# Kernel optimization log

Measured on AMD Instinct MI355X. Metric: run time of the kernel, lower is better.

Reference implementation:

```python
import jax, jax.numpy as jnp
import numpy as np

DIM, NH, HD = 512, 16, 32   # dim, num_heads, head_dim = dim // num_heads
WH, WW = 8, 8               # window_size
SCALE = HD ** -0.5


def _rope2(t):
    """Axial 2D rotary embedding. t: (M, WH, WW, HD). First HD/2 dims rotate
    with the height position, last HD/2 with the width position."""
    d = HD // 2
    inv_freq = 1.0 / (10000.0 ** (jnp.arange(0, d, 2, dtype=jnp.float32) / d))  # (d/2,)

    def cos_sin(n):
        ang = jnp.arange(n, dtype=jnp.float32)[:, None] * inv_freq              # (n, d/2)
        return (jnp.concatenate([jnp.cos(ang)] * 2, -1),
                jnp.concatenate([jnp.sin(ang)] * 2, -1))                        # (n, d)

    def rot_half(u):
        u1, u2 = jnp.split(u, 2, axis=-1)
        return jnp.concatenate([-u2, u1], -1)

    cos_h, sin_h = cos_sin(WH)
    cos_w, sin_w = cos_sin(WW)
    th, tw = t[..., :d], t[..., d:]
    th = th * cos_h[:, None, :] + rot_half(th) * sin_h[:, None, :]
    tw = tw * cos_w[None, :, :] + rot_half(tw) * sin_w[None, :, :]
    return jnp.concatenate([th, tw], -1)


def setup_inputs() -> dict:
    key = jax.random.key(0)
    ks = jax.random.split(key, 8)
    s = 0.02
    return {
        "x": jax.random.normal(ks[0], (8, 64, 64, DIM), dtype=jnp.float32),
        "qkv_w": jax.random.normal(ks[1], (DIM, 3 * DIM), dtype=jnp.float32) * s,
        "qkv_b": jnp.zeros((3 * DIM,), dtype=jnp.float32),
        "kv_w": jax.random.normal(ks[2], (DIM, 2 * DIM), dtype=jnp.float32) * s,
        "kv_b": jnp.zeros((2 * DIM,), dtype=jnp.float32),
        "proj_w": jax.random.normal(ks[3], (DIM, DIM), dtype=jnp.float32) * s,
        "proj_b": jnp.zeros((DIM,), dtype=jnp.float32),
    }


def reference(x, qkv_w, qkv_b, kv_w, kv_b, proj_w, proj_b):
    B, H, W, C = x.shape
    # --- hydra linear-attention branch (computed in the torch module even when
    # use_attn=True, but its result is discarded on that path) ---
    hy_k, hy_v = jnp.split(x @ kv_w + kv_b, 2, axis=-1)
    hy_k = hy_k / jnp.linalg.norm(hy_k, axis=-1, keepdims=True)
    hy_kv = (hy_k * hy_v).reshape(B, -1, C).sum(axis=-2, keepdims=True)  # (B,1,C), unused (use_attn=True)

    # --- window partition: (B,H,W,C) -> (B*nW, N, C), N = WH*WW ---
    xw = (x.reshape(B, H // WH, WH, W // WW, WW, C)
           .transpose(0, 1, 3, 2, 4, 5)
           .reshape(-1, WH * WW, C))
    B_, N, _ = xw.shape

    qkv = (xw @ qkv_w + qkv_b).reshape(B_, N, 3, NH, HD).transpose(2, 0, 3, 1, 4)
    q, k, v = qkv[0], qkv[1], qkv[2]                 # each (B_, NH, N, HD)

    q = _rope2(q.reshape(-1, WH, WW, HD)).reshape(B_, NH, N, HD)
    k = _rope2(k.reshape(-1, WH, WW, HD)).reshape(B_, NH, N, HD)

    attn = jax.nn.softmax(jnp.einsum('bhnd,bhmd->bhnm', q * SCALE, k), axis=-1)
    out = jnp.einsum('bhnm,bhmd->bhnd', attn, v)     # (B_, NH, N, HD)
    out = out.transpose(0, 2, 1, 3).reshape(B_, N, C)

    # --- window reverse: (B*nW, N, C) -> (B, H*W, C) ---
    out = (out.reshape(B, H // WH, W // WW, WH, WW, C)
              .transpose(0, 1, 3, 2, 4, 5)
              .reshape(B, H * W, C))

    out = out @ proj_w + proj_b
    return out.reshape(B, H, W, C)
```

## Files before the change

### kernel.cpp

```cpp
#include <hip/hip_runtime.h>
#include <cstdint>
#include <cstddef>

typedef float v4f  __attribute__((ext_vector_type(4)));
typedef __bf16 v8bf __attribute__((ext_vector_type(8)));
typedef __bf16 v4bf __attribute__((ext_vector_type(4)));

#define M_TOT 32768
#define KDIM  512
#define NQKV  1536
#define NPROJ 512

__device__ __constant__ float c_invf[8] = {
  1.f, 0.31622776601683794f, 0.1f, 0.031622776601683794f,
  0.01f, 0.0031622776601683794f, 0.001f, 0.00031622776601683794f };

__device__ __forceinline__ void async_copy16(const void* g, void* l) {
  __builtin_amdgcn_global_load_lds((const __attribute__((address_space(1))) void*)g,
                                   (__attribute__((address_space(3))) void*)l, 16, 0, 0);
}

__global__ void cast_x_kernel(const float* __restrict__ in, __bf16* __restrict__ out, int n8) {
  int i = blockIdx.x * blockDim.x + threadIdx.x;
  if (i >= n8) return;
  const float4* p = (const float4*)in + (size_t)i * 2;
  float4 a = p[0], b = p[1];
  v8bf r = { (__bf16)a.x, (__bf16)a.y, (__bf16)a.z, (__bf16)a.w,
             (__bf16)b.x, (__bf16)b.y, (__bf16)b.z, (__bf16)b.w };
  *(v8bf*)(out + (size_t)i * 8) = r;
}

__global__ __launch_bounds__(256) void transpose_cast_kernel(
    const float* __restrict__ w, __bf16* __restrict__ wt, int K, int N) {
  __shared__ __bf16 t[64 * 72];
  const int tid = threadIdx.x;
  const int n0 = blockIdx.x * 64, k0 = blockIdx.y * 64;
#pragma unroll
  for (int i = 0; i < 16; ++i) {
    int e = i * 256 + tid;
    int kk = e >> 6, nn = e & 63;
    t[nn * 72 + kk] = (__bf16)w[(size_t)(k0 + kk) * N + n0 + nn];
  }
  __syncthreads();
#pragma unroll
  for (int i = 0; i < 2; ++i) {
    int e = i * 256 + tid;
    int nn = e >> 3, kc = e & 7;
    *(v8bf*)&wt[(size_t)(n0 + nn) * K + k0 + kc * 8] = *(const v8bf*)&t[nn * 72 + kc * 8];
  }
}

#define QKV_OFF   28672
#define WIN_STRIDE 14848
#define QK_PITCH  40
#define V_PITCH   72

__global__ __launch_bounds__(256) void gemm_qkv_attn(
    const __bf16* __restrict__ A,
    const __bf16* __restrict__ Bt,
    const float* __restrict__ bias,
    __bf16* __restrict__ attn_out)
{
  __shared__ __align__(16) char smem[58368];
  __bf16* As = (__bf16*)smem;
  __bf16* Bs = (__bf16*)(smem + 16384);

  const int tid  = threadIdx.x;
  const int lane = tid & 63;
  const int wave = tid >> 6;
  const int lrow = lane & 15, quad = lane >> 4;
  const int head = blockIdx.y;

  int mbase[2];
#pragma unroll
  for (int l = 0; l < 2; ++l) {
    int w  = blockIdx.x * 2 + l;
    int b  = w >> 6, Wr = (w >> 3) & 7, Wc = w & 7;
    mbase[l] = b * 4096 + Wr * 512 + Wc * 8;
  }

  v4f acc[2][6] = {};

  for (int k0 = 0; k0 < KDIM; k0 += 64) {
#pragma unroll
    for (int i = 0; i < 4; ++i) {
      int s   = i * 256 + tid;
      int row = s >> 3, c = s & 7;
      int qc  = c ^ (row & 7);
      int tok = row & 63;
      int m   = mbase[row >> 6] + ((tok >> 3) << 6) + (tok & 7);
      async_copy16(A + (size_t)m * KDIM + k0 + qc * 8, &As[(i * 256 + (tid & ~63)) * 8]);
    }
#pragma unroll
    for (int i = 0; i < 3; ++i) {
      int s    = i * 256 + tid;
      int row  = s >> 3, c = s & 7;
      int qc   = c ^ (row & 7);
      int seg  = row >> 5;
      int grow = seg * 512 + head * 32 + (row & 31);
      async_copy16(Bt + (size_t)grow * KDIM + k0 + qc * 8, &Bs[(i * 256 + (tid & ~63)) * 8]);
    }
    __syncthreads();
#pragma unroll
    for (int kb = 0; kb < 2; ++kb) {
      int sx = (((kb << 2) | quad) ^ (lrow & 7)) * 8;
      v8bf af[2], bfr[6];
#pragma unroll
      for (int mi = 0; mi < 2; ++mi)
        af[mi] = *(const v8bf*)&As[(wave * 32 + mi * 16 + lrow) * 64 + sx];
#pragma unroll
      for (int ni = 0; ni < 6; ++ni)
        bfr[ni] = *(const v8bf*)&Bs[(ni * 16 + lrow) * 64 + sx];
#pragma unroll
      for (int mi = 0; mi < 2; ++mi)
#pragma unroll
        for (int ni = 0; ni < 6; ++ni)
          acc[mi][ni] = __builtin_amdgcn_mfma_f32_16x16x32_bf16(af[mi], bfr[ni], acc[mi][ni], 0, 0, 0);
    }
    __syncthreads();
  }

  const int wloc = wave & 1;
  const int win  = wave >> 1;
  __bf16* qL = (__bf16*)(smem + QKV_OFF + win * WIN_STRIDE);
  __bf16* kL = qL + 64 * QK_PITCH;
  __bf16* vL = kL + 64 * QK_PITCH;
  const int tokbase = 32 * wloc + quad * 4;

#pragma unroll
  for (int ni = 0; ni < 4; ++ni) {
    int c   = ni * 16 + lrow;
    int sel = c >> 5;
    int hd  = c & 31;
    float bv   = bias[sel * 512 + head * 32 + hd];
    float invf = c_invf[hd & 7];
    __bf16* dst = sel ? kL : qL;
#pragma unroll
    for (int mi = 0; mi < 2; ++mi) {
#pragma unroll
      for (int r = 0; r < 4; ++r) {
        int tok = tokbase + mi * 16 + r;
        float val = acc[mi][ni][r] + bv;
        float partner = __shfl_xor(val, 8);
        int p = (hd < 16) ? (tok >> 3) : (tok & 7);
        float ang = (float)p * invf;
        float sv, cv;
        __sincosf(ang, &sv, &cv);
        float rh = (hd & 8) ? partner : -partner;
        val = val * cv + rh * sv;
        if (sel == 0) val *= 0.17677669529663689f;
        dst[tok * QK_PITCH + hd] = (__bf16)val;
      }
    }
  }
#pragma unroll
  for (int ni = 4; ni < 6; ++ni) {
    int hd = (ni - 4) * 16 + lrow;
    float bv = bias[1024 + head * 32 + hd];
#pragma unroll
    for (int mi = 0; mi < 2; ++mi) {
      v4bf pk;
#pragma unroll
      for (int r = 0; r < 4; ++r) pk[r] = (__bf16)(acc[mi][ni][r] + bv);
      *(v4bf*)&vL[hd * V_PITCH + tokbase + mi * 16] = pk;
    }
  }
  __syncthreads();

  v8bf qf[2], kf[4];
#pragma unroll
  for (int mi = 0; mi < 2; ++mi)
    qf[mi] = *(const v8bf*)&qL[(32 * wloc + mi * 16 + lrow) * QK_PITCH + quad * 8];
#pragma unroll
  for (int ni = 0; ni < 4; ++ni)
    kf[ni] = *(const v8bf*)&kL[(ni * 16 + lrow) * QK_PITCH + quad * 8];

  v4f S[2][4] = {};
#pragma unroll
  for (int mi = 0; mi < 2; ++mi)
#pragma unroll
    for (int ni = 0; ni < 4; ++ni)
      S[mi][ni] = __builtin_amdgcn_mfma_f32_16x16x32_bf16(qf[mi], kf[ni], S[mi][ni], 0, 0, 0);

#pragma unroll
  for (int mi = 0; mi < 2; ++mi) {
#pragma unroll
    for (int r = 0; r < 4; ++r) {
      float mx = S[mi][0][r];
#pragma unroll
      for (int ni = 1; ni < 4; ++ni) mx = fmaxf(mx, S[mi][ni][r]);
      for (int d = 1; d < 16; d <<= 1) mx = fmaxf(mx, __shfl_xor(mx, d));
      float sum = 0.f;
#pragma unroll
      for (int ni = 0; ni < 4; ++ni) {
        float e = __expf(S[mi][ni][r] - mx);
        S[mi][ni][r] = e; sum += e;
      }
      for (int d = 1; d < 16; d <<= 1) sum += __shfl_xor(sum, d);
      float inv = 1.f / sum;
#pragma unroll
      for (int ni = 0; ni < 4; ++ni) S[mi][ni][r] *= inv;
    }
  }

  __bf16* Pw = (__bf16*)(smem + wave * 4608);
#pragma unroll
  for (int mi = 0; mi < 2; ++mi)
#pragma unroll
    for (int ni = 0; ni < 4; ++ni)
#pragma unroll
      for (int r = 0; r < 4; ++r)
        Pw[(mi * 16 + quad * 4 + r) * V_PITCH + ni * 16 + lrow] = (__bf16)S[mi][ni][r];
  __syncthreads();

  v8bf pf[2][2], vf[2][2];
#pragma unroll
  for (int mi = 0; mi < 2; ++mi)
#pragma unroll
    for (int kc = 0; kc < 2; ++kc)
      pf[mi][kc] = *(const v8bf*)&Pw[(mi * 16 + lrow) * V_PITCH + kc * 32 + quad * 8];
#pragma unroll
  for (int kc = 0; kc < 2; ++kc)
#pragma unroll
    for (int nj = 0; nj < 2; ++nj)
      vf[kc][nj] = *(const v8bf*)&vL[(nj * 16 + lrow) * V_PITCH + kc * 32 + quad * 8];

  v4f o[2][2] = {};
#pragma unroll
  for (int mi = 0; mi < 2; ++mi)
#pragma unroll
    for (int nj = 0; nj < 2; ++nj)
#pragma unroll
      for (int kc = 0; kc < 2; ++kc)
        o[mi][nj] = __builtin_amdgcn_mfma_f32_16x16x32_bf16(pf[mi][kc], vf[kc][nj], o[mi][nj], 0, 0, 0);

  const int gwin = blockIdx.x * 2 + win;
#pragma unroll
  for (int mi = 0; mi < 2; ++mi)
#pragma unroll
    for (int nj = 0; nj < 2; ++nj)
#pragma unroll
      for (int r = 0; r < 4; ++r) {
        int tok = 32 * wloc + mi * 16 + quad * 4 + r;
        int ch  = head * 32 + nj * 16 + lrow;
        attn_out[((size_t)gwin * 64 + tok) * 512 + ch] = (__bf16)o[mi][nj][r];
      }
}

__global__ __launch_bounds__(256) void gemm_proj(
    const __bf16* __restrict__ A,
    const __bf16* __restrict__ Bt,
    const float* __restrict__ bias,
    float* __restrict__ out)
{
  __shared__ __align__(16) char smem[32768];
  __bf16* As = (__bf16*)smem;
  __bf16* Bs = (__bf16*)(smem + 16384);
  const int tid  = threadIdx.x;
  const int lane = tid & 63;
  const int wave = tid >> 6;
  const int wm = wave >> 1, wn = wave & 1;
  const int m0 = blockIdx.x * 128, n0 = blockIdx.y * 128;
  const int lrow = lane & 15, quad = lane >> 4;

  v4f acc[4][4] = {};

  for (int k0 = 0; k0 < KDIM; k0 += 64) {
#pragma unroll
    for (int i = 0; i < 4; ++i) {
      int s   = i * 256 + tid;
      int row = s >> 3, c = s & 7;
      int q   = c ^ (row & 7);
      int wbase = (i * 256 + (tid & ~63)) * 8;
      async_copy16(A  + (size_t)(m0 + row) * KDIM + k0 + q * 8, &As[wbase]);
      async_copy16(Bt + (size_t)(n0 + row) * KDIM + k0 + q * 8, &Bs[wbase]);
    }
    __syncthreads();
#pragma unroll
    for (int kb = 0; kb < 2; ++kb) {
      int sx = (((kb << 2) | quad) ^ (lrow & 7)) * 8;
      v8bf af[4], bfr[4];
#pragma unroll
      for (int mi = 0; mi < 4; ++mi)
        af[mi] = *(const v8bf*)&As[(wm * 64 + mi * 16 + lrow) * 64 + sx];
#pragma unroll
      for (int ni = 0; ni < 4; ++ni)
        bfr[ni] = *(const v8bf*)&Bs[(wn * 64 + ni * 16 + lrow) * 64 + sx];
#pragma unroll
      for (int mi = 0; mi < 4; ++mi)
#pragma unroll
        for (int ni = 0; ni < 4; ++ni)
          acc[mi][ni] = __builtin_amdgcn_mfma_f32_16x16x32_bf16(af[mi], bfr[ni], acc[mi][ni], 0, 0, 0);
    }
    __syncthreads();
  }

  const int mb = m0 + wm * 64;
  const int nb = n0 + wn * 64;
#pragma unroll
  for (int ni = 0; ni < 4; ++ni) {
    int n = nb + ni * 16 + lrow;
    float bv = bias[n];
#pragma unroll
    for (int mi = 0; mi < 4; ++mi) {
#pragma unroll
      for (int r = 0; r < 4; ++r) {
        int m    = mb + mi * 16 + quad * 4 + r;
        int win  = m >> 6, tok = m & 63;
        int bb   = win >> 6;
        int hblk = (win >> 3) & 7, wblk = win & 7;
        int h    = hblk * 8 + (tok >> 3);
        int w    = wblk * 8 + (tok & 7);
        out[(((size_t)bb * 64 + h) * 64 + w) * 512 + n] = acc[mi][ni][r] + bv;
      }
    }
  }
}

extern "C" void kernel_launch(void* const* d_in, const int* in_sizes, int n_in,
                              void* d_out, int out_size, void* d_ws, size_t ws_size,
                              hipStream_t stream) {
  (void)in_sizes; (void)n_in; (void)out_size; (void)ws_size;
  const float* x      = (const float*)d_in[0];
  const float* qkv_w  = (const float*)d_in[1];
  const float* qkv_b  = (const float*)d_in[2];
  const float* proj_w = (const float*)d_in[5];
  const float* proj_b = (const float*)d_in[6];
  float* out = (float*)d_out;

  char* ws = (char*)d_ws;
  size_t off = 0;
  auto alloc = [&](size_t bytes) {
    char* p = ws + off;
    off += (bytes + 255) & ~(size_t)255;
    return (void*)p;
  };
  __bf16* xb       = (__bf16*)alloc((size_t)M_TOT * KDIM * 2);
  __bf16* qkv_wt   = (__bf16*)alloc((size_t)NQKV * KDIM * 2);
  __bf16* proj_wt  = (__bf16*)alloc((size_t)KDIM * KDIM * 2);
  __bf16* attn_out = (__bf16*)alloc((size_t)M_TOT * KDIM * 2);

  cast_x_kernel<<<dim3(M_TOT * KDIM / 8 / 256), dim3(256), 0, stream>>>(
      x, xb, M_TOT * KDIM / 8);
  transpose_cast_kernel<<<dim3(NQKV / 64, KDIM / 64), dim3(256), 0, stream>>>(
      qkv_w, qkv_wt, KDIM, NQKV);
  transpose_cast_kernel<<<dim3(NPROJ / 64, KDIM / 64), dim3(256), 0, stream>>>(
      proj_w, proj_wt, KDIM, NPROJ);

  gemm_qkv_attn<<<dim3(256, 16), dim3(256), 0, stream>>>(
      xb, qkv_wt, qkv_b, attn_out);

  gemm_proj<<<dim3(M_TOT / 128, NPROJ / 128), dim3(256), 0, stream>>>(
      attn_out, proj_wt, proj_b, out);
}
```

Measured before the change: 262.9 us.

## Enlarge per-wave tiles in QKV-attention and projection GEMMs, reorder grids

The fused QKV+attention kernel now covers two heads per block, with each wave owning a full 64-token window for one head. A wave computes a 64x96 tile instead of 32x96, and the block-wide syncs between the attention stages are removed because each wave uses its own LDS region. The projection GEMM moves to 256x128 tiles with each wave doing 64x128, and both grids are reordered so blocks that share weight tiles run close together. Global load addresses are precomputed and stepped by pointer increments. These changes raise MFMA work per LDS load and cut barriers, in exchange for more accumulator registers and larger LDS use, which may lower occupancy.

```diff
diff --git a/kernel.cpp b/kernel.cpp
--- a/kernel.cpp
+++ b/kernel.cpp
@@ -50,8 +50,7 @@
   }
 }
 
-#define QKV_OFF   28672
-#define WIN_STRIDE 14848
+#define REG_STRIDE 14848
 #define QK_PITCH  40
 #define V_PITCH   72
 
@@ -61,7 +60,7 @@
     const float* __restrict__ bias,
     __bf16* __restrict__ attn_out)
 {
-  __shared__ __align__(16) char smem[58368];
+  __shared__ __align__(16) char smem[59392];
   __bf16* As = (__bf16*)smem;
   __bf16* Bs = (__bf16*)(smem + 16384);
 
@@ -69,78 +68,85 @@
   const int lane = tid & 63;
   const int wave = tid >> 6;
   const int lrow = lane & 15, quad = lane >> 4;
-  const int head = blockIdx.y;
+  const int hp   = blockIdx.x;
+  const int mt   = blockIdx.y;
+  const int wl   = wave >> 1, hl = wave & 1;
+  const int head = hp * 2 + hl;
 
   int mbase[2];
 #pragma unroll
   for (int l = 0; l < 2; ++l) {
-    int w  = blockIdx.x * 2 + l;
+    int w  = mt * 2 + l;
     int b  = w >> 6, Wr = (w >> 3) & 7, Wc = w & 7;
     mbase[l] = b * 4096 + Wr * 512 + Wc * 8;
   }
 
-  v4f acc[2][6] = {};
+  const __bf16* aptr[4]; __bf16* adst[4];
+  const __bf16* bptr[6]; __bf16* bdst[6];
+#pragma unroll
+  for (int i = 0; i < 4; ++i) {
+    int s = i * 256 + tid;
+    int row = s >> 3, c = s & 7, qc = c ^ (row & 7);
+    int tok = row & 63;
+    int m = mbase[row >> 6] + ((tok >> 3) << 6) + (tok & 7);
+    aptr[i] = A + (size_t)m * KDIM + qc * 8;
+    adst[i] = &As[(i * 256 + (tid & ~63)) * 8];
+  }
+#pragma unroll
+  for (int i = 0; i < 6; ++i) {
+    int s = i * 256 + tid;
+    int rl = s >> 3, c = s & 7, qc = c ^ (rl & 7);
+    int sel = rl >> 6, rem = rl & 63;
+    int grow = sel * 512 + (hp * 2 + (rem >> 5)) * 32 + (rem & 31);
+    bptr[i] = Bt + (size_t)grow * KDIM + qc * 8;
+    bdst[i] = &Bs[(i * 256 + (tid & ~63)) * 8];
+  }
+
+  v4f acc[4][6] = {};
 
   for (int k0 = 0; k0 < KDIM; k0 += 64) {
 #pragma unroll
-    for (int i = 0; i < 4; ++i) {
-      int s   = i * 256 + tid;
-      int row = s >> 3, c = s & 7;
-      int qc  = c ^ (row & 7);
-      int tok = row & 63;
-      int m   = mbase[row >> 6] + ((tok >> 3) << 6) + (tok & 7);
-      async_copy16(A + (size_t)m * KDIM + k0 + qc * 8, &As[(i * 256 + (tid & ~63)) * 8]);
-    }
-#pragma unroll
-    for (int i = 0; i < 3; ++i) {
-      int s    = i * 256 + tid;
-      int row  = s >> 3, c = s & 7;
-      int qc   = c ^ (row & 7);
-      int seg  = row >> 5;
-      int grow = seg * 512 + head * 32 + (row & 31);
-      async_copy16(Bt + (size_t)grow * KDIM + k0 + qc * 8, &Bs[(i * 256 + (tid & ~63)) * 8]);
-    }
+    for (int i = 0; i < 4; ++i) { async_copy16(aptr[i], adst[i]); aptr[i] += 64; }
+#pragma unroll
+    for (int i = 0; i < 6; ++i) { async_copy16(bptr[i], bdst[i]); bptr[i] += 64; }
     __syncthreads();
 #pragma unroll
     for (int kb = 0; kb < 2; ++kb) {
       int sx = (((kb << 2) | quad) ^ (lrow & 7)) * 8;
-      v8bf af[2], bfr[6];
-#pragma unroll
-      for (int mi = 0; mi < 2; ++mi)
-        af[mi] = *(const v8bf*)&As[(wave * 32 + mi * 16 + lrow) * 64 + sx];
-#pragma unroll
-      for (int ni = 0; ni < 6; ++ni)
-        bfr[ni] = *(const v8bf*)&Bs[(ni * 16 + lrow) * 64 + sx];
-#pragma unroll
-      for (int mi = 0; mi < 2; ++mi)
-#pragma unroll
-        for (int ni = 0; ni < 6; ++ni)
-          acc[mi][ni] = __builtin_amdgcn_mfma_f32_16x16x32_bf16(af[mi], bfr[ni], acc[mi][ni], 0, 0, 0);
+      v8bf af[4], bfr[6];
+#pragma unroll
+      for (int mi = 0; mi < 4; ++mi)
+        af[mi] = *(const v8bf*)&As[(wl * 64 + mi * 16 + lrow) * 64 + sx];
+#pragma unroll
+      for (int j = 0; j < 6; ++j)
+        bfr[j] = *(const v8bf*)&Bs[((j >> 1) * 64 + hl * 32 + (j & 1) * 16 + lrow) * 64 + sx];
+#pragma unroll
+      for (int mi = 0; mi < 4; ++mi)
+#pragma unroll
+        for (int j = 0; j < 6; ++j)
+          acc[mi][j] = __builtin_amdgcn_mfma_f32_16x16x32_bf16(af[mi], bfr[j], acc[mi][j], 0, 0, 0);
     }
     __syncthreads();
   }
 
-  const int wloc = wave & 1;
-  const int win  = wave >> 1;
-  __bf16* qL = (__bf16*)(smem + QKV_OFF + win * WIN_STRIDE);
-  __bf16* kL = qL + 64 * QK_PITCH;
+  __bf16* reg = (__bf16*)(smem + wave * REG_STRIDE);
+  __bf16* qL = reg;
+  __bf16* kL = reg + 64 * QK_PITCH;
   __bf16* vL = kL + 64 * QK_PITCH;
-  const int tokbase = 32 * wloc + quad * 4;
-
-#pragma unroll
-  for (int ni = 0; ni < 4; ++ni) {
-    int c   = ni * 16 + lrow;
-    int sel = c >> 5;
-    int hd  = c & 31;
+
+#pragma unroll
+  for (int j = 0; j < 4; ++j) {
+    int sel = j >> 1, nh = j & 1;
+    int hd  = nh * 16 + lrow;
     float bv   = bias[sel * 512 + head * 32 + hd];
     float invf = c_invf[hd & 7];
     __bf16* dst = sel ? kL : qL;
 #pragma unroll
-    for (int mi = 0; mi < 2; ++mi) {
+    for (int mi = 0; mi < 4; ++mi) {
 #pragma unroll
       for (int r = 0; r < 4; ++r) {
-        int tok = tokbase + mi * 16 + r;
-        float val = acc[mi][ni][r] + bv;
+        int tok = mi * 16 + quad * 4 + r;
+        float val = acc[mi][j][r] + bv;
         float partner = __shfl_xor(val, 8);
         int p = (hd < 16) ? (tok >> 3) : (tok & 7);
         float ang = (float)p * invf;
@@ -154,36 +160,35 @@
     }
   }
 #pragma unroll
-  for (int ni = 4; ni < 6; ++ni) {
-    int hd = (ni - 4) * 16 + lrow;
+  for (int j = 4; j < 6; ++j) {
+    int hd = (j - 4) * 16 + lrow;
     float bv = bias[1024 + head * 32 + hd];
 #pragma unroll
-    for (int mi = 0; mi < 2; ++mi) {
+    for (int mi = 0; mi < 4; ++mi) {
       v4bf pk;
 #pragma unroll
-      for (int r = 0; r < 4; ++r) pk[r] = (__bf16)(acc[mi][ni][r] + bv);
-      *(v4bf*)&vL[hd * V_PITCH + tokbase + mi * 16] = pk;
-    }
-  }
-  __syncthreads();
-
-  v8bf qf[2], kf[4];
-#pragma unroll
-  for (int mi = 0; mi < 2; ++mi)
-    qf[mi] = *(const v8bf*)&qL[(32 * wloc + mi * 16 + lrow) * QK_PITCH + quad * 8];
+      for (int r = 0; r < 4; ++r) pk[r] = (__bf16)(acc[mi][j][r] + bv);
+      *(v4bf*)&vL[hd * V_PITCH + mi * 16 + quad * 4] = pk;
+    }
+  }
+
+  v8bf qf[4], kf[4];
+#pragma unroll
+  for (int mi = 0; mi < 4; ++mi)
+    qf[mi] = *(const v8bf*)&qL[(mi * 16 + lrow) * QK_PITCH + quad * 8];
 #pragma unroll
   for (int ni = 0; ni < 4; ++ni)
     kf[ni] = *(const v8bf*)&kL[(ni * 16 + lrow) * QK_PITCH + quad * 8];
 
-  v4f S[2][4] = {};
-#pragma unroll
-  for (int mi = 0; mi < 2; ++mi)
+  v4f S[4][4] = {};
+#pragma unroll
+  for (int mi = 0; mi < 4; ++mi)
 #pragma unroll
     for (int ni = 0; ni < 4; ++ni)
       S[mi][ni] = __builtin_amdgcn_mfma_f32_16x16x32_bf16(qf[mi], kf[ni], S[mi][ni], 0, 0, 0);
 
 #pragma unroll
-  for (int mi = 0; mi < 2; ++mi) {
+  for (int mi = 0; mi < 4; ++mi) {
 #pragma unroll
     for (int r = 0; r < 4; ++r) {
       float mx = S[mi][0][r];
@@ -203,45 +208,44 @@
     }
   }
 
-  __bf16* Pw = (__bf16*)(smem + wave * 4608);
-#pragma unroll
-  for (int mi = 0; mi < 2; ++mi)
+  __bf16* P = reg;
+#pragma unroll
+  for (int mi = 0; mi < 4; ++mi)
 #pragma unroll
     for (int ni = 0; ni < 4; ++ni)
 #pragma unroll
       for (int r = 0; r < 4; ++r)
-        Pw[(mi * 16 + quad * 4 + r) * V_PITCH + ni * 16 + lrow] = (__bf16)S[mi][ni][r];
-  __syncthreads();
-
-  v8bf pf[2][2], vf[2][2];
-#pragma unroll
-  for (int mi = 0; mi < 2; ++mi)
+        P[(mi * 16 + quad * 4 + r) * V_PITCH + ni * 16 + lrow] = (__bf16)S[mi][ni][r];
+
+  v8bf pf[4][2], vf[2][2];
+#pragma unroll
+  for (int mi = 0; mi < 4; ++mi)
 #pragma unroll
     for (int kc = 0; kc < 2; ++kc)
-      pf[mi][kc] = *(const v8bf*)&Pw[(mi * 16 + lrow) * V_PITCH + kc * 32 + quad * 8];
+      pf[mi][kc] = *(const v8bf*)&P[(mi * 16 + lrow) * V_PITCH + kc * 32 + quad * 8];
 #pragma unroll
   for (int kc = 0; kc < 2; ++kc)
 #pragma unroll
     for (int nj = 0; nj < 2; ++nj)
       vf[kc][nj] = *(const v8bf*)&vL[(nj * 16 + lrow) * V_PITCH + kc * 32 + quad * 8];
 
-  v4f o[2][2] = {};
-#pragma unroll
-  for (int mi = 0; mi < 2; ++mi)
+  v4f o[4][2] = {};
+#pragma unroll
+  for (int mi = 0; mi < 4; ++mi)
 #pragma unroll
     for (int nj = 0; nj < 2; ++nj)
 #pragma unroll
       for (int kc = 0; kc < 2; ++kc)
         o[mi][nj] = __builtin_amdgcn_mfma_f32_16x16x32_bf16(pf[mi][kc], vf[kc][nj], o[mi][nj], 0, 0, 0);
 
-  const int gwin = blockIdx.x * 2 + win;
-#pragma unroll
-  for (int mi = 0; mi < 2; ++mi)
+  const int gwin = mt * 2 + wl;
+#pragma unroll
+  for (int mi = 0; mi < 4; ++mi)
 #pragma unroll
     for (int nj = 0; nj < 2; ++nj)
 #pragma unroll
       for (int r = 0; r < 4; ++r) {
-        int tok = 32 * wloc + mi * 16 + quad * 4 + r;
+        int tok = mi * 16 + quad * 4 + r;
         int ch  = head * 32 + nj * 16 + lrow;
         attn_out[((size_t)gwin * 64 + tok) * 512 + ch] = (__bf16)o[mi][nj][r];
       }
@@ -253,53 +257,63 @@
     const float* __restrict__ bias,
     float* __restrict__ out)
 {
-  __shared__ __align__(16) char smem[32768];
+  __shared__ __align__(16) char smem[49152];
   __bf16* As = (__bf16*)smem;
-  __bf16* Bs = (__bf16*)(smem + 16384);
+  __bf16* Bs = (__bf16*)(smem + 32768);
   const int tid  = threadIdx.x;
   const int lane = tid & 63;
   const int wave = tid >> 6;
-  const int wm = wave >> 1, wn = wave & 1;
-  const int m0 = blockIdx.x * 128, n0 = blockIdx.y * 128;
+  const int n0 = blockIdx.x * 128, m0 = blockIdx.y * 256;
   const int lrow = lane & 15, quad = lane >> 4;
 
-  v4f acc[4][4] = {};
+  const __bf16* aptr[8]; __bf16* adst[8];
+  const __bf16* bptr[4]; __bf16* bdst[4];
+#pragma unroll
+  for (int i = 0; i < 8; ++i) {
+    int s = i * 256 + tid;
+    int row = s >> 3, c = s & 7, qc = c ^ (row & 7);
+    aptr[i] = A + (size_t)(m0 + row) * KDIM + qc * 8;
+    adst[i] = &As[(i * 256 + (tid & ~63)) * 8];
+  }
+#pragma unroll
+  for (int i = 0; i < 4; ++i) {
+    int s = i * 256 + tid;
+    int row = s >> 3, c = s & 7, qc = c ^ (row & 7);
+    bptr[i] = Bt + (size_t)(n0 + row) * KDIM + qc * 8;
+    bdst[i] = &Bs[(i * 256 + (tid & ~63)) * 8];
+  }
+
+  v4f acc[4][8] = {};
 
   for (int k0 = 0; k0 < KDIM; k0 += 64) {
 #pragma unroll
-    for (int i = 0; i < 4; ++i) {
-      int s   = i * 256 + tid;
-      int row = s >> 3, c = s & 7;
-      int q   = c ^ (row & 7);
-      int wbase = (i * 256 + (tid & ~63)) * 8;
-      async_copy16(A  + (size_t)(m0 + row) * KDIM + k0 + q * 8, &As[wbase]);
-      async_copy16(Bt + (size_t)(n0 + row) * KDIM + k0 + q * 8, &Bs[wbase]);
-    }
+    for (int i = 0; i < 8; ++i) { async_copy16(aptr[i], adst[i]); aptr[i] += 64; }
+#pragma unroll
+    for (int i = 0; i < 4; ++i) { async_copy16(bptr[i], bdst[i]); bptr[i] += 64; }
     __syncthreads();
 #pragma unroll
     for (int kb = 0; kb < 2; ++kb) {
       int sx = (((kb << 2) | quad) ^ (lrow & 7)) * 8;
-      v8bf af[4], bfr[4];
+      v8bf af[4], bfr[8];
 #pragma unroll
       for (int mi = 0; mi < 4; ++mi)
-        af[mi] = *(const v8bf*)&As[(wm * 64 + mi * 16 + lrow) * 64 + sx];
-#pragma unroll
-      for (int ni = 0; ni < 4; ++ni)
-        bfr[ni] = *(const v8bf*)&Bs[(wn * 64 + ni * 16 + lrow) * 64 + sx];
+        af[mi] = *(const v8bf*)&As[(wave * 64 + mi * 16 + lrow) * 64 + sx];
+#pragma unroll
+      for (int ni = 0; ni < 8; ++ni)
+        bfr[ni] = *(const v8bf*)&Bs[(ni * 16 + lrow) * 64 + sx];
 #pragma unroll
       for (int mi = 0; mi < 4; ++mi)
 #pragma unroll
-        for (int ni = 0; ni < 4; ++ni)
+        for (int ni = 0; ni < 8; ++ni)
           acc[mi][ni] = __builtin_amdgcn_mfma_f32_16x16x32_bf16(af[mi], bfr[ni], acc[mi][ni], 0, 0, 0);
     }
     __syncthreads();
   }
 
-  const int mb = m0 + wm * 64;
-  const int nb = n0 + wn * 64;
-#pragma unroll
-  for (int ni = 0; ni < 4; ++ni) {
-    int n = nb + ni * 16 + lrow;
+  const int mb = m0 + wave * 64;
+#pragma unroll
+  for (int ni = 0; ni < 8; ++ni) {
+    int n = n0 + ni * 16 + lrow;
     float bv = bias[n];
 #pragma unroll
     for (int mi = 0; mi < 4; ++mi) {
@@ -347,9 +361,9 @@
   transpose_cast_kernel<<<dim3(NPROJ / 64, KDIM / 64), dim3(256), 0, stream>>>(
       proj_w, proj_wt, KDIM, NPROJ);
 
-  gemm_qkv_attn<<<dim3(256, 16), dim3(256), 0, stream>>>(
+  gemm_qkv_attn<<<dim3(8, 256), dim3(256), 0, stream>>>(
       xb, qkv_wt, qkv_b, attn_out);
 
-  gemm_proj<<<dim3(M_TOT / 128, NPROJ / 128), dim3(256), 0, stream>>>(
+  gemm_proj<<<dim3(4, 128), dim3(256), 0, stream>>>(
       attn_out, proj_wt, proj_b, out);
 }
```

After: 262.0 us. No clear change (-0.3%).
